# Optimization experiments

Measured on AMD Instinct MI355X. Metric: run time of the kernel, lower is better.

The kernel has to match this reference:

```python
import jax, jax.numpy as jnp
import numpy as np

B, L = 4, 40960
C = 512
DMLP = 2048
TEMP = 1e-5
EPS = 1e-5
FACTOR = 2  # Smartpool factor at layer 4


def setup_inputs() -> dict:
    key = jax.random.key(0)
    ks = jax.random.split(key, 8)

    def w(k, shape, fan_in):
        return jax.random.normal(k, shape, jnp.float32) / np.float32(np.sqrt(fan_in))

    inp = {
        "x": jax.random.normal(ks[0], (B, 1, L), jnp.float32),
        "conv0_w": w(ks[1], (C, 1, 10), 10),   "conv0_b": jnp.zeros(C, jnp.float32),
        "conv1_w": w(ks[2], (C, C, 8), C * 8), "conv1_b": jnp.zeros(C, jnp.float32),
        "conv2_w": w(ks[3], (C, C, 4), C * 4), "conv2_b": jnp.zeros(C, jnp.float32),
        "conv3_w": w(ks[4], (C, C, 4), C * 4), "conv3_b": jnp.zeros(C, jnp.float32),
        "mlp_w1": w(ks[5], (C, DMLP), C),       "mlp_b1": jnp.zeros(DMLP, jnp.float32),
        "mlp_w2": w(ks[6], (DMLP, DMLP), DMLP), "mlp_b2": jnp.zeros(DMLP, jnp.float32),
        "mlp_w3": w(ks[7], (DMLP, 1), DMLP),    "mlp_b3": jnp.zeros(1, jnp.float32),
    }
    for i in range(5):  # ChannelNorm affine params (init: ones/zeros)
        inp[f"n{i}_w"] = jnp.ones(C, jnp.float32)
        inp[f"n{i}_b"] = jnp.zeros(C, jnp.float32)
    return inp


def _conv(x, w, b, stride, pad):
    # Conv1d with padding_mode='reflect': reflect-pad then VALID conv. x: [B,C,T]
    x = jnp.pad(x, ((0, 0), (0, 0), (pad, pad)), mode="reflect")
    y = jax.lax.conv_general_dilated(x, w, (stride,), "VALID",
                                     dimension_numbers=("NCH", "OIH", "NCH"))
    return y + b[None, :, None]


def _cnorm(x, g, b):
    # ChannelNorm: normalize over channel dim with unbiased variance (torch.var default)
    m = jnp.mean(x, axis=1, keepdims=True)
    v = jnp.var(x, axis=1, keepdims=True, ddof=1)
    return (x - m) * jax.lax.rsqrt(v + EPS) * g[None, :, None] + b[None, :, None]


def _forward(x, conv0_w, conv0_b, conv1_w, conv1_b, conv2_w, conv2_b, conv3_w, conv3_b,
             n0_w, n0_b, n1_w, n1_b, n2_w, n2_b, n3_w, n3_b, n4_w, n4_b,
             mlp_w1, mlp_b1, mlp_w2, mlp_b2, mlp_w3, mlp_b3):
    h = jax.nn.relu(_cnorm(_conv(x, conv0_w, conv0_b, 5, 3), n0_w, n0_b))
    h = jax.nn.relu(_cnorm(_conv(h, conv1_w, conv1_b, 4, 2), n1_w, n1_b))
    h = jax.nn.relu(_cnorm(_conv(h, conv2_w, conv2_b, 2, 1), n2_w, n2_b))
    h = jax.nn.relu(_cnorm(_conv(h, conv3_w, conv3_b, 2, 1), n3_w, n3_b))

    f = jnp.transpose(h, (0, 2, 1))  # [B,T,C]
    T = f.shape[1]

    # importance MLP (dropout inactive in eval), exact GELU, sigmoid head
    z = jax.nn.gelu(f @ mlp_w1 + mlp_b1, approximate=False)
    z = jax.nn.gelu(z @ mlp_w2 + mlp_b2, approximate=False)
    imp = jax.nn.sigmoid((z @ mlp_w3 + mlp_b3)[..., 0]) + TEMP          # [B,T]
    imp = imp / jnp.sum(imp, axis=1, keepdims=True) * (T / FACTOR)      # sums to T/factor

    # warp: cumsum -> ramp contributions -> 2x2 [[-1,1],[1,-1]] conv = double diff
    Tn = T // FACTOR  # == round(importance_cs[0,-1])
    cs = jnp.cumsum(imp, axis=1)                                        # [B,T]
    p = jnp.maximum(cs[:, :, None] - jnp.arange(Tn, dtype=cs.dtype)[None, None, :], 0.0)  # [B,T,Tn]
    pc = jnp.pad(p, ((0, 0), (0, 0), (0, 1)))
    d = pc[:, :, :-1] - pc[:, :, 1:]                                    # diff along new-time axis
    wmat = d - jnp.pad(d, ((0, 0), (1, 0), (0, 0)))[:, :-1, :]          # diff along old-time axis, [B,T,Tn]
    pooled = jnp.einsum("btn,btc->bnc", wmat, f)                        # interp_weights @ X

    out = jnp.transpose(pooled, (0, 2, 1))                              # [B,C,Tn]
    return jax.nn.relu(_cnorm(out, n4_w, n4_b))


def reference(x, conv0_w, conv0_b, conv1_w, conv1_b, conv2_w, conv2_b, conv3_w, conv3_b,
              n0_w, n0_b, n1_w, n1_b, n2_w, n2_b, n3_w, n3_b, n4_w, n4_b,
              mlp_w1, mlp_b1, mlp_w2, mlp_b2, mlp_w3, mlp_b3):
    return _forward(x, conv0_w, conv0_b, conv1_w, conv1_b, conv2_w, conv2_b, conv3_w, conv3_b,
                    n0_w, n0_b, n1_w, n1_b, n2_w, n2_b, n3_w, n3_b, n4_w, n4_b,
                    mlp_w1, mlp_b1, mlp_w2, mlp_b2, mlp_w3, mlp_b3)
```

## Files before the change

### kernel.cpp

```cpp
#include <hip/hip_runtime.h>
#include <hip/hip_bf16.h>
#include <math.h>

#define NB 4
#define LIN 40960
#define NC 512
#define T0 8192
#define T1 2048
#define T2 1024
#define T3 512
#define TN 256
#define DM 2048
#define EPSF 1e-5f
#define TEMPF 1e-5f

typedef __attribute__((ext_vector_type(8))) short bf16x8;
typedef __attribute__((ext_vector_type(4))) float f32x4;

__device__ __forceinline__ int refl(int t, int T) {
  if (t < 0) t = -t;
  if (t >= T) t = 2 * T - 2 - t;
  return t;
}

__device__ __forceinline__ void gld16(void* lds, const void* g) {
  __builtin_amdgcn_global_load_lds((const __attribute__((address_space(1))) unsigned int*)g,
                                   (__attribute__((address_space(3))) unsigned int*)lds, 16, 0, 0);
}

__device__ __forceinline__ void blk_sum2_512(float& a, float& b, float* scratch) {
#pragma unroll
  for (int off = 32; off > 0; off >>= 1) {
    a += __shfl_down(a, off, 64);
    b += __shfl_down(b, off, 64);
  }
  int lane = threadIdx.x & 63, wid = threadIdx.x >> 6;
  __syncthreads();
  if (lane == 0) { scratch[wid] = a; scratch[8 + wid] = b; }
  __syncthreads();
  float sa = 0.f, sb = 0.f;
#pragma unroll
  for (int i = 0; i < 8; i++) { sa += scratch[i]; sb += scratch[8 + i]; }
  a = sa; b = sb;
}

__device__ __forceinline__ void add_bf8(const __hip_bfloat16* p, float* v) {
  union { uint4 u; __hip_bfloat16 h[8]; } pk;
  pk.u = *(const uint4*)p;
#pragma unroll
  for (int j = 0; j < 8; j++) v[j] += __bfloat162float(pk.h[j]);
}

template <int KT>
__device__ __forceinline__ void prep_conv_body(const float* __restrict__ w, __hip_bfloat16* __restrict__ wt,
                                               int co, float* l) {
  const float* wb = w + (size_t)co * 512 * KT;
  for (int i = threadIdx.x; i < 512 * KT; i += 256) l[i] = wb[i];
  __syncthreads();
  __hip_bfloat16* wo = wt + (size_t)co * 512 * KT;
  for (int i = threadIdx.x; i < 512 * KT; i += 256) {
    int kk = i >> 9, ci = i & 511;
    wo[i] = __float2bfloat16(l[ci * KT + kk]);
  }
}

template <int KD, int ND>
__device__ __forceinline__ void prep_mlp_body(const float* __restrict__ w, __hip_bfloat16* __restrict__ wt,
                                              int bidx, float* sbuf) {
  float(*tile)[33] = (float(*)[33])sbuf;
  int bx = bidx % (ND / 32);
  int by = bidx / (ND / 32);
  int tx = threadIdx.x & 31, ty = threadIdx.x >> 5;
#pragma unroll
  for (int i = 0; i < 32; i += 8)
    tile[ty + i][tx] = w[(size_t)(by * 32 + ty + i) * ND + bx * 32 + tx];
  __syncthreads();
#pragma unroll
  for (int i = 0; i < 32; i += 8)
    wt[(size_t)(bx * 32 + ty + i) * KD + by * 32 + tx] = __float2bfloat16(tile[tx][ty + i]);
}

__global__ __launch_bounds__(256) void k_prep(const float* c1w, const float* c2w, const float* c3w,
                                              const float* mw1, const float* mw2,
                                              __hip_bfloat16* wt1, __hip_bfloat16* wt2,
                                              __hip_bfloat16* wt3, __hip_bfloat16* wm1t,
                                              __hip_bfloat16* wm2t) {
  __shared__ float sb[4096];
  int b = blockIdx.x;
  if (b < 512) prep_conv_body<8>(c1w, wt1, b, sb);
  else if (b < 1024) prep_conv_body<4>(c2w, wt2, b - 512, sb);
  else if (b < 1536) prep_conv_body<4>(c3w, wt3, b - 1024, sb);
  else if (b < 2560) prep_mlp_body<512, 2048>(mw1, wm1t, b - 1536, sb);
  else prep_mlp_body<2048, 2048>(mw2, wm2t, b - 2560, sb);
}

__global__ __launch_bounds__(512) void k_conv0(const float* __restrict__ x, const float* __restrict__ w,
                                               const float* __restrict__ bias, const float* __restrict__ gw,
                                               const float* __restrict__ gb, __hip_bfloat16* __restrict__ out) {
  __shared__ float xv[48];
  __shared__ float tb[512 * 9];
  __shared__ float stats[16];
  int b = blockIdx.x / (T0 / 8);
  int t0 = (blockIdx.x % (T0 / 8)) * 8;
  int tid = threadIdx.x;
  if (tid < 45) xv[tid] = x[(size_t)b * LIN + refl(t0 * 5 - 3 + tid, LIN)];
  __syncthreads();
  float wk[10];
#pragma unroll
  for (int k = 0; k < 10; k++) wk[k] = w[tid * 10 + k];
  float bs = bias[tid];
  float acc[8];
#pragma unroll
  for (int tt = 0; tt < 8; tt++) {
    float a = bs;
#pragma unroll
    for (int k = 0; k < 10; k++) a += xv[tt * 5 + k] * wk[k];
    acc[tt] = a;
    tb[tid * 9 + tt] = a;
  }
  __syncthreads();
  int wave = tid >> 6, lane = tid & 63;
  float s = 0.f, q = 0.f;
#pragma unroll
  for (int j = 0; j < 8; j++) {
    float v = tb[(lane * 8 + j) * 9 + wave];
    s += v; q += v * v;
  }
#pragma unroll
  for (int off = 32; off > 0; off >>= 1) {
    s += __shfl_xor(s, off, 64);
    q += __shfl_xor(q, off, 64);
  }
  if (lane == 0) {
    float mean = s * (1.f / NC);
    float var = fmaxf((q - s * s * (1.f / NC)) * (1.f / (NC - 1)), 0.f);
    stats[wave] = mean;
    stats[8 + wave] = rsqrtf(var + EPSF);
  }
  __syncthreads();
  float gwv = gw[tid], gbv = gb[tid];
#pragma unroll
  for (int tt = 0; tt < 8; tt++) {
    float y = (acc[tt] - stats[tt]) * stats[8 + tt] * gwv + gbv;
    out[((size_t)(b * T0 + t0 + tt)) * NC + tid] = __float2bfloat16(fmaxf(y, 0.f));
  }
}

template <int MODE, int TIN_, int TOUT_, int SS, int PP, int KK, int NN, int SPLITK, int MM>
__global__ __launch_bounds__(256, 2) void k_gemm2(const __hip_bfloat16* __restrict__ A,
                                                  const __hip_bfloat16* __restrict__ Bt,
                                                  __hip_bfloat16* __restrict__ Cp) {
  __shared__ __align__(16) __hip_bfloat16 sA[2][256 * 32];
  __shared__ __align__(16) __hip_bfloat16 sB[2][128 * 32];
  const int tid = threadIdx.x;
  const int lane = tid & 63;
  const int wave = tid >> 6;
  const int wm = wave >> 1, wn = wave & 1;
  constexpr int nt = NN / 128;
  constexpr int PS = (MM / 2048) * nt;
  constexpr int KBT = KK / 32;
  const int blk = blockIdx.x;
  const int xs = blk & 7, sl = blk >> 3;
  const int sk = sl / PS, rem = sl % PS;
  const int row0 = ((rem / nt) * 8 + xs) * 256;
  const int col0 = (rem % nt) * 128;
  const int kb0 = (sk * KBT) / SPLITK, kb1 = ((sk + 1) * KBT) / SPLITK;
  const int cq = lane >> 4, cl = lane & 15;

  const char* aP[4];
  const char* bP[2];

  auto stage = [&](int kb, int buf) {
    bool recalc = (kb == kb0) || (MODE == 1 && (kb & 15) == 0);
    if (recalc) {
#pragma unroll
      for (int rr = 0; rr < 4; rr++) {
        int c = rr * 256 + tid;
        int m = c >> 2, kc = c & 3;
        int kcs = kc ^ (m & 3);
        size_t ga;
        if (MODE == 0) {
          ga = (size_t)(row0 + m) * KK + kb * 32 + kcs * 8;
        } else {
          int r = row0 + m;
          int bb = r / TOUT_;
          int t = r - bb * TOUT_;
          int k = (kb * 32) >> 9;
          int ci = ((kb * 32) & 511) + kcs * 8;
          int gt = refl(t * SS - PP + k, TIN_);
          ga = (((size_t)(bb * TIN_ + gt)) << 9) + ci;
        }
        aP[rr] = (const char*)(A + ga);
      }
#pragma unroll
      for (int rr = 0; rr < 2; rr++) {
        int c = rr * 256 + tid;
        int n = c >> 2, kc = c & 3;
        int kcs = kc ^ (n & 3);
        bP[rr] = (const char*)(Bt + (size_t)(col0 + n) * KK + kb * 32 + kcs * 8);
      }
    }
#pragma unroll
    for (int rr = 0; rr < 4; rr++) {
      int c = rr * 256 + tid;
      gld16((char*)&sA[buf][0] + c * 16, aP[rr]);
      aP[rr] += 64;
    }
#pragma unroll
    for (int rr = 0; rr < 2; rr++) {
      int c = rr * 256 + tid;
      gld16((char*)&sB[buf][0] + c * 16, bP[rr]);
      bP[rr] += 64;
    }
  };

  f32x4 acc[8][4];
  const f32x4 zz = {0.f, 0.f, 0.f, 0.f};
#pragma unroll
  for (int mi = 0; mi < 8; mi++)
#pragma unroll
    for (int ni = 0; ni < 4; ni++) acc[mi][ni] = zz;

  stage(kb0, 0);
  const int p = cq ^ (cl & 3);
  for (int kb = kb0; kb < kb1; kb++) {
    int cur = (kb - kb0) & 1;
    __syncthreads();
    if (kb + 1 < kb1) stage(kb + 1, cur ^ 1);
    const short* bA = (const short*)&sA[cur][0];
    const short* bB = (const short*)&sB[cur][0];
    bf16x8 af[8], bfr[4];
#pragma unroll
    for (int mi = 0; mi < 8; mi++)
      af[mi] = *(const bf16x8*)(bA + (wm * 128 + mi * 16 + cl) * 32 + p * 8);
#pragma unroll
    for (int ni = 0; ni < 4; ni++)
      bfr[ni] = *(const bf16x8*)(bB + (wn * 64 + ni * 16 + cl) * 32 + p * 8);
#pragma unroll
    for (int mi = 0; mi < 8; mi++)
#pragma unroll
      for (int ni = 0; ni < 4; ni++)
        acc[mi][ni] = __builtin_amdgcn_mfma_f32_16x16x32_bf16(af[mi], bfr[ni], acc[mi][ni], 0, 0, 0);
  }

#pragma unroll
  for (int mi = 0; mi < 8; mi++)
#pragma unroll
    for (int ni = 0; ni < 4; ni++)
#pragma unroll
      for (int r2 = 0; r2 < 4; r2++) {
        int row = row0 + wm * 128 + mi * 16 + cq * 4 + r2;
        int col = col0 + wn * 64 + ni * 16 + cl;
        Cp[(size_t)sk * MM * NN + (size_t)row * NN + col] = __float2bfloat16(acc[mi][ni][r2]);
      }
}

template <int MODE, int TIN_, int TOUT_, int SS, int PP, int KK, int NN, int EPI, int SPLITK, int MM>
__global__ __launch_bounds__(256, 4) void k_gemm(const __hip_bfloat16* __restrict__ A,
                                                 const __hip_bfloat16* __restrict__ Bt,
                                                 const float* __restrict__ bias,
                                                 __hip_bfloat16* __restrict__ Cout) {
  __shared__ __align__(16) __hip_bfloat16 sA[2][64 * 32];
  __shared__ __align__(16) __hip_bfloat16 sB[2][128 * 32];
  const int tid = threadIdx.x;
  const int lane = tid & 63;
  const int wave = tid >> 6;
  const int wm = wave >> 1, wn = wave & 1;
  constexpr int nt = NN / 128;
  constexpr int PS = (MM / 512) * nt;
  constexpr int KBT = KK / 32;
  const int blk = blockIdx.x;
  const int xs = blk & 7, sl = blk >> 3;
  const int sk = sl / PS, rem = sl % PS;
  const int row0 = ((rem / nt) * 8 + xs) * 64;
  const int col0 = (rem % nt) * 128;
  const int kb0 = (sk * KBT) / SPLITK, kb1 = ((sk + 1) * KBT) / SPLITK;
  const int cq = lane >> 4, cl = lane & 15;

  const char* aP;
  const char* bP[2];

  auto stage = [&](int kb, int buf) {
    bool recalc = (kb == kb0) || (MODE == 1 && (kb & 15) == 0);
    if (recalc) {
      {
        int m = tid >> 2, kc = tid & 3;
        int kcs = kc ^ (m & 3);
        size_t ga;
        if (MODE == 0) {
          ga = (size_t)(row0 + m) * KK + kb * 32 + kcs * 8;
        } else {
          int r = row0 + m;
          int bb = r / TOUT_;
          int t = r - bb * TOUT_;
          int k = (kb * 32) >> 9;
          int ci = ((kb * 32) & 511) + kcs * 8;
          int gt = refl(t * SS - PP + k, TIN_);
          ga = (((size_t)(bb * TIN_ + gt)) << 9) + ci;
        }
        aP = (const char*)(A + ga);
      }
#pragma unroll
      for (int rr = 0; rr < 2; rr++) {
        int c = rr * 256 + tid;
        int n = c >> 2, kc = c & 3;
        int kcs = kc ^ (n & 3);
        bP[rr] = (const char*)(Bt + (size_t)(col0 + n) * KK + kb * 32 + kcs * 8);
      }
    }
    gld16((char*)&sA[buf][0] + tid * 16, aP);
    aP += 64;
#pragma unroll
    for (int rr = 0; rr < 2; rr++) {
      int c = rr * 256 + tid;
      gld16((char*)&sB[buf][0] + c * 16, bP[rr]);
      bP[rr] += 64;
    }
  };

  f32x4 acc[2][4];
  const f32x4 zz = {0.f, 0.f, 0.f, 0.f};
#pragma unroll
  for (int mi = 0; mi < 2; mi++)
#pragma unroll
    for (int ni = 0; ni < 4; ni++) acc[mi][ni] = zz;

  stage(kb0, 0);
  const int p = cq ^ (cl & 3);
  for (int kb = kb0; kb < kb1; kb++) {
    int cur = (kb - kb0) & 1;
    __syncthreads();
    if (kb + 1 < kb1) stage(kb + 1, cur ^ 1);
    const short* bA = (const short*)&sA[cur][0];
    const short* bB = (const short*)&sB[cur][0];
    bf16x8 af[2], bfr[4];
#pragma unroll
    for (int mi = 0; mi < 2; mi++)
      af[mi] = *(const bf16x8*)(bA + (wm * 32 + mi * 16 + cl) * 32 + p * 8);
#pragma unroll
    for (int ni = 0; ni < 4; ni++)
      bfr[ni] = *(const bf16x8*)(bB + (wn * 64 + ni * 16 + cl) * 32 + p * 8);
#pragma unroll
    for (int mi = 0; mi < 2; mi++)
#pragma unroll
      for (int ni = 0; ni < 4; ni++)
        acc[mi][ni] = __builtin_amdgcn_mfma_f32_16x16x32_bf16(af[mi], bfr[ni], acc[mi][ni], 0, 0, 0);
  }

#pragma unroll
  for (int mi = 0; mi < 2; mi++)
#pragma unroll
    for (int ni = 0; ni < 4; ni++)
#pragma unroll
      for (int r2 = 0; r2 < 4; r2++) {
        int row = row0 + wm * 32 + mi * 16 + cq * 4 + r2;
        int col = col0 + wn * 64 + ni * 16 + cl;
        float v = acc[mi][ni][r2];
        if (EPI == 1) {
          v += bias[col];
          v = 0.5f * v * (1.f + erff(v * 0.70710678118654752f));
          Cout[(size_t)row * NN + col] = __float2bfloat16(v);
        } else {
          Cout[(size_t)sk * MM * NN + (size_t)row * NN + col] = __float2bfloat16(v);
        }
      }
}

template <int NS>
__global__ __launch_bounds__(512) void k_cnorm(const __hip_bfloat16* __restrict__ g,
                                               const float* __restrict__ cb,
                                               const float* __restrict__ gw, const float* __restrict__ gb,
                                               __hip_bfloat16* __restrict__ out, size_t stride) {
  int wave = threadIdx.x >> 6, lane = threadIdx.x & 63;
  size_t row = (size_t)blockIdx.x * 8 + wave;
  float v[8];
  {
    float4 c0 = *(const float4*)(cb + lane * 8), c1 = *(const float4*)(cb + lane * 8 + 4);
    v[0] = c0.x; v[1] = c0.y; v[2] = c0.z; v[3] = c0.w;
    v[4] = c1.x; v[5] = c1.y; v[6] = c1.z; v[7] = c1.w;
  }
#pragma unroll
  for (int s = 0; s < NS; s++) add_bf8(g + s * stride + row * NC + lane * 8, v);
  float s = 0.f, q = 0.f;
#pragma unroll
  for (int j = 0; j < 8; j++) { s += v[j]; q += v[j] * v[j]; }
#pragma unroll
  for (int off = 32; off > 0; off >>= 1) {
    s += __shfl_xor(s, off, 64);
    q += __shfl_xor(q, off, 64);
  }
  float mean = s * (1.f / NC);
  float var = fmaxf((q - s * s * (1.f / NC)) * (1.f / (NC - 1)), 0.f);
  float rstd = rsqrtf(var + EPSF);
  float4 w0 = *(const float4*)(gw + lane * 8), w1 = *(const float4*)(gw + lane * 8 + 4);
  float4 b0 = *(const float4*)(gb + lane * 8), b1 = *(const float4*)(gb + lane * 8 + 4);
  float gwv[8] = {w0.x, w0.y, w0.z, w0.w, w1.x, w1.y, w1.z, w1.w};
  float gbv[8] = {b0.x, b0.y, b0.z, b0.w, b1.x, b1.y, b1.z, b1.w};
  union { __hip_bfloat16 h[8]; uint4 u; } pk;
#pragma unroll
  for (int j = 0; j < 8; j++)
    pk.h[j] = __float2bfloat16(fmaxf((v[j] - mean) * rstd * gwv[j] + gbv[j], 0.f));
  *(uint4*)(out + row * NC + lane * 8) = pk.u;
}

template <int NS>
__global__ __launch_bounds__(256) void k_head(const __hip_bfloat16* __restrict__ g,
                                              const float* __restrict__ b2,
                                              const float* __restrict__ w3, const float* __restrict__ b3,
                                              float* __restrict__ imp) {
  __shared__ float red[4];
  int row = blockIdx.x, tid = threadIdx.x;
  int c = tid * 8;
  float v[8];
  {
    float4 x0 = *(const float4*)(b2 + c), x1 = *(const float4*)(b2 + c + 4);
    v[0] = x0.x; v[1] = x0.y; v[2] = x0.z; v[3] = x0.w;
    v[4] = x1.x; v[5] = x1.y; v[6] = x1.z; v[7] = x1.w;
  }
#pragma unroll
  for (int s = 0; s < NS; s++) add_bf8(g + (size_t)s * (2048 * DM) + (size_t)row * DM + c, v);
  float a = 0.f;
  float4 w0 = *(const float4*)(w3 + c), w1 = *(const float4*)(w3 + c + 4);
  float wv[8] = {w0.x, w0.y, w0.z, w0.w, w1.x, w1.y, w1.z, w1.w};
#pragma unroll
  for (int j = 0; j < 8; j++) {
    float z = 0.5f * v[j] * (1.f + erff(v[j] * 0.70710678118654752f));
    a += z * wv[j];
  }
#pragma unroll
  for (int off = 32; off > 0; off >>= 1) a += __shfl_down(a, off, 64);
  int lane = tid & 63, wid = tid >> 6;
  if (lane == 0) red[wid] = a;
  __syncthreads();
  if (tid == 0) {
    float s = red[0] + red[1] + red[2] + red[3] + b3[0];
    imp[row] = 1.f / (1.f + expf(-s)) + TEMPF;
  }
}

__device__ __forceinline__ float dfun(float cv, int n) {
  float d = fmaxf(cv - (float)n, 0.f);
  if (n < TN - 1) d = fminf(d, 1.f);
  return d;
}

__global__ __launch_bounds__(512) void k_poolfinal(const __hip_bfloat16* __restrict__ f,
                                                   const float* __restrict__ imp,
                                                   const float* __restrict__ gw, const float* __restrict__ gb,
                                                   float* __restrict__ out) {
  __shared__ float wt[T3];
  __shared__ float wsum[8];
  __shared__ float red[16];
  int b = blockIdx.x / TN, n = blockIdx.x % TN;
  int tid = threadIdx.x, wave = tid >> 6, lane = tid & 63;
  float own = imp[b * T3 + tid];
  float s = own;
#pragma unroll
  for (int off = 1; off < 64; off <<= 1) {
    float t = __shfl_up(s, off, 64);
    if (lane >= off) s += t;
  }
  if (lane == 63) wsum[wave] = s;
  __syncthreads();
  float prefix = 0.f, total = 0.f;
#pragma unroll
  for (int w = 0; w < 8; w++) {
    float ws_ = wsum[w];
    total += ws_;
    if (w < wave) prefix += ws_;
  }
  float scale = (float)TN / total;
  float incl = (prefix + s) * scale;
  float excl = (prefix + s - own) * scale;
  wt[tid] = dfun(incl, n) - dfun(excl, n);
  __syncthreads();
  float acc = 0.f;
  for (int t = 0; t < T3; t++) {
    float w = wt[t];
    if (w != 0.f) acc += w * __bfloat162float(f[((size_t)b * T3 + t) * NC + tid]);
  }
  float sv = acc, q = acc * acc;
  blk_sum2_512(sv, q, red);
  float mean = sv * (1.f / NC);
  float var = fmaxf((q - sv * sv * (1.f / NC)) * (1.f / (NC - 1)), 0.f);
  float y = (acc - mean) * rsqrtf(var + EPSF) * gw[tid] + gb[tid];
  out[((size_t)b * NC + tid) * TN + n] = fmaxf(y, 0.f);
}

extern "C" void kernel_launch(void* const* d_in, const int* in_sizes, int n_in,
                              void* d_out, int out_size, void* d_ws, size_t ws_size,
                              hipStream_t stream) {
  const float* x   = (const float*)d_in[0];
  const float* c0w = (const float*)d_in[1];  const float* c0b = (const float*)d_in[2];
  const float* c1w = (const float*)d_in[3];  const float* c1b = (const float*)d_in[4];
  const float* c2w = (const float*)d_in[5];  const float* c2b = (const float*)d_in[6];
  const float* c3w = (const float*)d_in[7];  const float* c3b = (const float*)d_in[8];
  const float* mw1 = (const float*)d_in[9];  const float* mb1 = (const float*)d_in[10];
  const float* mw2 = (const float*)d_in[11]; const float* mb2 = (const float*)d_in[12];
  const float* mw3 = (const float*)d_in[13]; const float* mb3 = (const float*)d_in[14];
  const float* n0w = (const float*)d_in[15]; const float* n0b = (const float*)d_in[16];
  const float* n1w = (const float*)d_in[17]; const float* n1b = (const float*)d_in[18];
  const float* n2w = (const float*)d_in[19]; const float* n2b = (const float*)d_in[20];
  const float* n3w = (const float*)d_in[21]; const float* n3b = (const float*)d_in[22];
  const float* n4w = (const float*)d_in[23]; const float* n4b = (const float*)d_in[24];

  char* base = (char*)d_ws;
  __hip_bfloat16* h0b  = (__hip_bfloat16*)(base);
  __hip_bfloat16* h1b  = (__hip_bfloat16*)(base);
  __hip_bfloat16* h2b  = (__hip_bfloat16*)(base + (8u << 20));
  __hip_bfloat16* h3b  = (__hip_bfloat16*)(base + (12u << 20));
  __hip_bfloat16* z1b  = (__hip_bfloat16*)(base + (14u << 20));
  float*          imp  = (float*)(base + (22u << 20));
  __hip_bfloat16* g    = (__hip_bfloat16*)(base + (32u << 20));
  __hip_bfloat16* wm1t = (__hip_bfloat16*)(base + (64u << 20));
  __hip_bfloat16* wt2  = (__hip_bfloat16*)(base + (66u << 20));
  __hip_bfloat16* wt3  = (__hip_bfloat16*)(base + (68u << 20));
  __hip_bfloat16* wt1  = (__hip_bfloat16*)(base + (70u << 20));
  __hip_bfloat16* wm2t = (__hip_bfloat16*)(base + (74u << 20));
  float* outp = (float*)d_out;

  k_prep<<<6656, 256, 0, stream>>>(c1w, c2w, c3w, mw1, mw2, wt1, wt2, wt3, wm1t, wm2t);
  k_conv0<<<NB * (T0 / 8), 512, 0, stream>>>(x, c0w, c0b, n0w, n0b, h0b);

  k_gemm2<1, 8192, 2048, 4, 2, 4096, 512, 4, 8192><<<512, 256, 0, stream>>>(h0b, wt1, g);
  k_cnorm<4><<<8192 / 8, 512, 0, stream>>>(g, c1b, n1w, n1b, h1b, (size_t)8192 * 512);
  k_gemm2<1, 2048, 1024, 2, 1, 2048, 512, 8, 4096><<<512, 256, 0, stream>>>(h1b, wt2, g);
  k_cnorm<8><<<4096 / 8, 512, 0, stream>>>(g, c2b, n2w, n2b, h2b, (size_t)4096 * 512);
  k_gemm<1, 1024, 512, 2, 1, 2048, 512, 0, 8, 2048><<<1024, 256, 0, stream>>>(h2b, wt3, nullptr, g);
  k_cnorm<8><<<2048 / 8, 512, 0, stream>>>(g, c3b, n3w, n3b, h3b, (size_t)2048 * 512);

  k_gemm<0, 0, 1, 0, 0, 512, 2048, 1, 1, 2048><<<512, 256, 0, stream>>>(h3b, wm1t, mb1, z1b);
  k_gemm2<0, 0, 1, 0, 0, 2048, 2048, 4, 2048><<<512, 256, 0, stream>>>(z1b, wm2t, g);

  k_head<4><<<NB * T3, 256, 0, stream>>>(g, mb2, mw3, mb3, imp);
  k_poolfinal<<<NB * TN, 512, 0, stream>>>(h3b, imp, n4w, n4b, outp);
}
```

Measured before the change: 323.7 us.

## Fuse channel-norm and MLP head into split-K GEMM tails via last-block counters

The weight prep and conv0 kernels are merged into one launch. The separate channel-norm and head kernels are removed. Each split-K GEMM now uses per-row-group atomic counters so that the last finishing block reduces the partials and applies bias, channel norm and ReLU, or the GELU/dot/sigmoid head. This cuts kernel launches and the gaps between them, at the cost of a serialized tail run by a few blocks, extra fences, and a memset for the counters.

```diff
diff --git a/kernel.cpp b/kernel.cpp
--- a/kernel.cpp
+++ b/kernel.cpp
@@ -55,10 +55,10 @@
 __device__ __forceinline__ void prep_conv_body(const float* __restrict__ w, __hip_bfloat16* __restrict__ wt,
                                                int co, float* l) {
   const float* wb = w + (size_t)co * 512 * KT;
-  for (int i = threadIdx.x; i < 512 * KT; i += 256) l[i] = wb[i];
+  for (int i = threadIdx.x; i < 512 * KT; i += 512) l[i] = wb[i];
   __syncthreads();
   __hip_bfloat16* wo = wt + (size_t)co * 512 * KT;
-  for (int i = threadIdx.x; i < 512 * KT; i += 256) {
+  for (int i = threadIdx.x; i < 512 * KT; i += 512) {
     int kk = i >> 9, ci = i & 511;
     wo[i] = __float2bfloat16(l[ci * KT + kk]);
   }
@@ -72,36 +72,23 @@
   int by = bidx / (ND / 32);
   int tx = threadIdx.x & 31, ty = threadIdx.x >> 5;
 #pragma unroll
-  for (int i = 0; i < 32; i += 8)
+  for (int i = 0; i < 32; i += 16)
     tile[ty + i][tx] = w[(size_t)(by * 32 + ty + i) * ND + bx * 32 + tx];
   __syncthreads();
 #pragma unroll
-  for (int i = 0; i < 32; i += 8)
+  for (int i = 0; i < 32; i += 16)
     wt[(size_t)(bx * 32 + ty + i) * KD + by * 32 + tx] = __float2bfloat16(tile[tx][ty + i]);
 }
 
-__global__ __launch_bounds__(256) void k_prep(const float* c1w, const float* c2w, const float* c3w,
-                                              const float* mw1, const float* mw2,
-                                              __hip_bfloat16* wt1, __hip_bfloat16* wt2,
-                                              __hip_bfloat16* wt3, __hip_bfloat16* wm1t,
-                                              __hip_bfloat16* wm2t) {
-  __shared__ float sb[4096];
-  int b = blockIdx.x;
-  if (b < 512) prep_conv_body<8>(c1w, wt1, b, sb);
-  else if (b < 1024) prep_conv_body<4>(c2w, wt2, b - 512, sb);
-  else if (b < 1536) prep_conv_body<4>(c3w, wt3, b - 1024, sb);
-  else if (b < 2560) prep_mlp_body<512, 2048>(mw1, wm1t, b - 1536, sb);
-  else prep_mlp_body<2048, 2048>(mw2, wm2t, b - 2560, sb);
-}
-
-__global__ __launch_bounds__(512) void k_conv0(const float* __restrict__ x, const float* __restrict__ w,
-                                               const float* __restrict__ bias, const float* __restrict__ gw,
-                                               const float* __restrict__ gb, __hip_bfloat16* __restrict__ out) {
-  __shared__ float xv[48];
-  __shared__ float tb[512 * 9];
-  __shared__ float stats[16];
-  int b = blockIdx.x / (T0 / 8);
-  int t0 = (blockIdx.x % (T0 / 8)) * 8;
+__device__ __forceinline__ void conv0_body(const float* __restrict__ x, const float* __restrict__ w,
+                                           const float* __restrict__ bias, const float* __restrict__ gw,
+                                           const float* __restrict__ gb, __hip_bfloat16* __restrict__ out,
+                                           int blk, float* smem) {
+  float* xv = smem;
+  float* tb = smem + 64;
+  float* stats = smem + 4672;
+  int b = blk / (T0 / 8);
+  int t0 = (blk % (T0 / 8)) * 8;
   int tid = threadIdx.x;
   if (tid < 45) xv[tid] = x[(size_t)b * LIN + refl(t0 * 5 - 3 + tid, LIN)];
   __syncthreads();
@@ -146,10 +133,33 @@
   }
 }
 
-template <int MODE, int TIN_, int TOUT_, int SS, int PP, int KK, int NN, int SPLITK, int MM>
+__global__ __launch_bounds__(512) void k_init(const float* x, const float* c0w, const float* c0b,
+                                              const float* n0w, const float* n0b, __hip_bfloat16* h0b,
+                                              const float* c1w, const float* c2w, const float* c3w,
+                                              const float* mw1, const float* mw2,
+                                              __hip_bfloat16* wt1, __hip_bfloat16* wt2,
+                                              __hip_bfloat16* wt3, __hip_bfloat16* wm1t,
+                                              __hip_bfloat16* wm2t) {
+  __shared__ float smem[4688];
+  int b = blockIdx.x;
+  if (b < 4096) conv0_body(x, c0w, c0b, n0w, n0b, h0b, b, smem);
+  else if (b < 4608) prep_conv_body<8>(c1w, wt1, b - 4096, smem);
+  else if (b < 5120) prep_conv_body<4>(c2w, wt2, b - 4608, smem);
+  else if (b < 5632) prep_conv_body<4>(c3w, wt3, b - 5120, smem);
+  else if (b < 6656) prep_mlp_body<512, 2048>(mw1, wm1t, b - 5632, smem);
+  else prep_mlp_body<2048, 2048>(mw2, wm2t, b - 6656, smem);
+}
+
+template <int MODE, int TIN_, int TOUT_, int SS, int PP, int KK, int NN, int SPLITK, int MM, int FIN>
 __global__ __launch_bounds__(256, 2) void k_gemm2(const __hip_bfloat16* __restrict__ A,
                                                   const __hip_bfloat16* __restrict__ Bt,
-                                                  __hip_bfloat16* __restrict__ Cp) {
+                                                  __hip_bfloat16* __restrict__ Cp,
+                                                  int* __restrict__ cnt,
+                                                  const float* __restrict__ f0,
+                                                  const float* __restrict__ f1,
+                                                  const float* __restrict__ f2,
+                                                  __hip_bfloat16* __restrict__ outB,
+                                                  float* __restrict__ outF) {
   __shared__ __align__(16) __hip_bfloat16 sA[2][256 * 32];
   __shared__ __align__(16) __hip_bfloat16 sB[2][128 * 32];
   const int tid = threadIdx.x;
@@ -162,7 +172,8 @@
   const int blk = blockIdx.x;
   const int xs = blk & 7, sl = blk >> 3;
   const int sk = sl / PS, rem = sl % PS;
-  const int row0 = ((rem / nt) * 8 + xs) * 256;
+  const int rg = (rem / nt) * 8 + xs;
+  const int row0 = rg * 256;
   const int col0 = (rem % nt) * 128;
   const int kb0 = (sk * KBT) / SPLITK, kb1 = ((sk + 1) * KBT) / SPLITK;
   const int cq = lane >> 4, cl = lane & 15;
@@ -253,13 +264,83 @@
         int col = col0 + wn * 64 + ni * 16 + cl;
         Cp[(size_t)sk * MM * NN + (size_t)row * NN + col] = __float2bfloat16(acc[mi][ni][r2]);
       }
-}
-
-template <int MODE, int TIN_, int TOUT_, int SS, int PP, int KK, int NN, int EPI, int SPLITK, int MM>
+
+  if constexpr (FIN != 0) {
+    __threadfence();
+    __shared__ int lf;
+    if (tid == 0) lf = (atomicAdd(cnt + rg, 1) == nt * SPLITK - 1) ? 1 : 0;
+    __syncthreads();
+    if (!lf) return;
+    __threadfence();
+    if constexpr (FIN == 1) {
+      float4 c0 = *(const float4*)(f0 + lane * 8), c1 = *(const float4*)(f0 + lane * 8 + 4);
+      float4 w0 = *(const float4*)(f1 + lane * 8), w1 = *(const float4*)(f1 + lane * 8 + 4);
+      float4 b0 = *(const float4*)(f2 + lane * 8), b1 = *(const float4*)(f2 + lane * 8 + 4);
+      float cbv[8] = {c0.x, c0.y, c0.z, c0.w, c1.x, c1.y, c1.z, c1.w};
+      float gwv[8] = {w0.x, w0.y, w0.z, w0.w, w1.x, w1.y, w1.z, w1.w};
+      float gbv[8] = {b0.x, b0.y, b0.z, b0.w, b1.x, b1.y, b1.z, b1.w};
+      for (int it = 0; it < 64; it++) {
+        int row = row0 + it * 4 + wave;
+        float v[8];
+#pragma unroll
+        for (int j = 0; j < 8; j++) v[j] = cbv[j];
+#pragma unroll
+        for (int s = 0; s < SPLITK; s++)
+          add_bf8(Cp + (size_t)s * MM * NN + (size_t)row * NN + lane * 8, v);
+        float s1 = 0.f, q = 0.f;
+#pragma unroll
+        for (int j = 0; j < 8; j++) { s1 += v[j]; q += v[j] * v[j]; }
+#pragma unroll
+        for (int off = 32; off > 0; off >>= 1) {
+          s1 += __shfl_xor(s1, off, 64);
+          q += __shfl_xor(q, off, 64);
+        }
+        float mean = s1 * (1.f / NC);
+        float var = fmaxf((q - s1 * s1 * (1.f / NC)) * (1.f / (NC - 1)), 0.f);
+        float rstd = rsqrtf(var + EPSF);
+        union { __hip_bfloat16 h[8]; uint4 u; } pk;
+#pragma unroll
+        for (int j = 0; j < 8; j++)
+          pk.h[j] = __float2bfloat16(fmaxf((v[j] - mean) * rstd * gwv[j] + gbv[j], 0.f));
+        *(uint4*)(outB + (size_t)row * NN + lane * 8) = pk.u;
+      }
+    } else {
+      for (int it = 0; it < 64; it++) {
+        int row = row0 + it * 4 + wave;
+        float a = 0.f;
+#pragma unroll
+        for (int gq = 0; gq < 4; gq++) {
+          int c = gq * 512 + lane * 8;
+          float4 x0 = *(const float4*)(f0 + c), x1 = *(const float4*)(f0 + c + 4);
+          float v[8] = {x0.x, x0.y, x0.z, x0.w, x1.x, x1.y, x1.z, x1.w};
+#pragma unroll
+          for (int s = 0; s < SPLITK; s++)
+            add_bf8(Cp + (size_t)s * MM * NN + (size_t)row * NN + c, v);
+          float4 y0 = *(const float4*)(f1 + c), y1 = *(const float4*)(f1 + c + 4);
+          float wv[8] = {y0.x, y0.y, y0.z, y0.w, y1.x, y1.y, y1.z, y1.w};
+#pragma unroll
+          for (int j = 0; j < 8; j++) {
+            float z = 0.5f * v[j] * (1.f + erff(v[j] * 0.70710678118654752f));
+            a += z * wv[j];
+          }
+        }
+#pragma unroll
+        for (int off = 32; off > 0; off >>= 1) a += __shfl_down(a, off, 64);
+        if (lane == 0) outF[row] = 1.f / (1.f + expf(-(a + f2[0]))) + TEMPF;
+      }
+    }
+  }
+}
+
+template <int MODE, int TIN_, int TOUT_, int SS, int PP, int KK, int NN, int EPI, int SPLITK, int MM, int FIN>
 __global__ __launch_bounds__(256, 4) void k_gemm(const __hip_bfloat16* __restrict__ A,
                                                  const __hip_bfloat16* __restrict__ Bt,
                                                  const float* __restrict__ bias,
-                                                 __hip_bfloat16* __restrict__ Cout) {
+                                                 __hip_bfloat16* __restrict__ Cout,
+                                                 int* __restrict__ cnt,
+                                                 const float* __restrict__ f1,
+                                                 const float* __restrict__ f2,
+                                                 __hip_bfloat16* __restrict__ outB) {
   __shared__ __align__(16) __hip_bfloat16 sA[2][64 * 32];
   __shared__ __align__(16) __hip_bfloat16 sB[2][128 * 32];
   const int tid = threadIdx.x;
@@ -272,7 +353,8 @@
   const int blk = blockIdx.x;
   const int xs = blk & 7, sl = blk >> 3;
   const int sk = sl / PS, rem = sl % PS;
-  const int row0 = ((rem / nt) * 8 + xs) * 64;
+  const int rg = (rem / nt) * 8 + xs;
+  const int row0 = rg * 64;
   const int col0 = (rem % nt) * 128;
   const int kb0 = (sk * KBT) / SPLITK, kb1 = ((sk + 1) * KBT) / SPLITK;
   const int cq = lane >> 4, cl = lane & 15;
@@ -364,77 +446,45 @@
           Cout[(size_t)sk * MM * NN + (size_t)row * NN + col] = __float2bfloat16(v);
         }
       }
-}
-
-template <int NS>
-__global__ __launch_bounds__(512) void k_cnorm(const __hip_bfloat16* __restrict__ g,
-                                               const float* __restrict__ cb,
-                                               const float* __restrict__ gw, const float* __restrict__ gb,
-                                               __hip_bfloat16* __restrict__ out, size_t stride) {
-  int wave = threadIdx.x >> 6, lane = threadIdx.x & 63;
-  size_t row = (size_t)blockIdx.x * 8 + wave;
-  float v[8];
-  {
-    float4 c0 = *(const float4*)(cb + lane * 8), c1 = *(const float4*)(cb + lane * 8 + 4);
-    v[0] = c0.x; v[1] = c0.y; v[2] = c0.z; v[3] = c0.w;
-    v[4] = c1.x; v[5] = c1.y; v[6] = c1.z; v[7] = c1.w;
-  }
-#pragma unroll
-  for (int s = 0; s < NS; s++) add_bf8(g + s * stride + row * NC + lane * 8, v);
-  float s = 0.f, q = 0.f;
-#pragma unroll
-  for (int j = 0; j < 8; j++) { s += v[j]; q += v[j] * v[j]; }
-#pragma unroll
-  for (int off = 32; off > 0; off >>= 1) {
-    s += __shfl_xor(s, off, 64);
-    q += __shfl_xor(q, off, 64);
-  }
-  float mean = s * (1.f / NC);
-  float var = fmaxf((q - s * s * (1.f / NC)) * (1.f / (NC - 1)), 0.f);
-  float rstd = rsqrtf(var + EPSF);
-  float4 w0 = *(const float4*)(gw + lane * 8), w1 = *(const float4*)(gw + lane * 8 + 4);
-  float4 b0 = *(const float4*)(gb + lane * 8), b1 = *(const float4*)(gb + lane * 8 + 4);
-  float gwv[8] = {w0.x, w0.y, w0.z, w0.w, w1.x, w1.y, w1.z, w1.w};
-  float gbv[8] = {b0.x, b0.y, b0.z, b0.w, b1.x, b1.y, b1.z, b1.w};
-  union { __hip_bfloat16 h[8]; uint4 u; } pk;
-#pragma unroll
-  for (int j = 0; j < 8; j++)
-    pk.h[j] = __float2bfloat16(fmaxf((v[j] - mean) * rstd * gwv[j] + gbv[j], 0.f));
-  *(uint4*)(out + row * NC + lane * 8) = pk.u;
-}
-
-template <int NS>
-__global__ __launch_bounds__(256) void k_head(const __hip_bfloat16* __restrict__ g,
-                                              const float* __restrict__ b2,
-                                              const float* __restrict__ w3, const float* __restrict__ b3,
-                                              float* __restrict__ imp) {
-  __shared__ float red[4];
-  int row = blockIdx.x, tid = threadIdx.x;
-  int c = tid * 8;
-  float v[8];
-  {
-    float4 x0 = *(const float4*)(b2 + c), x1 = *(const float4*)(b2 + c + 4);
-    v[0] = x0.x; v[1] = x0.y; v[2] = x0.z; v[3] = x0.w;
-    v[4] = x1.x; v[5] = x1.y; v[6] = x1.z; v[7] = x1.w;
-  }
-#pragma unroll
-  for (int s = 0; s < NS; s++) add_bf8(g + (size_t)s * (2048 * DM) + (size_t)row * DM + c, v);
-  float a = 0.f;
-  float4 w0 = *(const float4*)(w3 + c), w1 = *(const float4*)(w3 + c + 4);
-  float wv[8] = {w0.x, w0.y, w0.z, w0.w, w1.x, w1.y, w1.z, w1.w};
-#pragma unroll
-  for (int j = 0; j < 8; j++) {
-    float z = 0.5f * v[j] * (1.f + erff(v[j] * 0.70710678118654752f));
-    a += z * wv[j];
-  }
-#pragma unroll
-  for (int off = 32; off > 0; off >>= 1) a += __shfl_down(a, off, 64);
-  int lane = tid & 63, wid = tid >> 6;
-  if (lane == 0) red[wid] = a;
-  __syncthreads();
-  if (tid == 0) {
-    float s = red[0] + red[1] + red[2] + red[3] + b3[0];
-    imp[row] = 1.f / (1.f + expf(-s)) + TEMPF;
+
+  if constexpr (FIN == 1) {
+    __threadfence();
+    __shared__ int lf;
+    if (tid == 0) lf = (atomicAdd(cnt + rg, 1) == nt * SPLITK - 1) ? 1 : 0;
+    __syncthreads();
+    if (!lf) return;
+    __threadfence();
+    float4 c0 = *(const float4*)(bias + lane * 8), c1 = *(const float4*)(bias + lane * 8 + 4);
+    float4 w0 = *(const float4*)(f1 + lane * 8), w1 = *(const float4*)(f1 + lane * 8 + 4);
+    float4 b0 = *(const float4*)(f2 + lane * 8), b1 = *(const float4*)(f2 + lane * 8 + 4);
+    float cbv[8] = {c0.x, c0.y, c0.z, c0.w, c1.x, c1.y, c1.z, c1.w};
+    float gwv[8] = {w0.x, w0.y, w0.z, w0.w, w1.x, w1.y, w1.z, w1.w};
+    float gbv[8] = {b0.x, b0.y, b0.z, b0.w, b1.x, b1.y, b1.z, b1.w};
+    for (int it = 0; it < 16; it++) {
+      int row = row0 + it * 4 + wave;
+      float v[8];
+#pragma unroll
+      for (int j = 0; j < 8; j++) v[j] = cbv[j];
+#pragma unroll
+      for (int s = 0; s < SPLITK; s++)
+        add_bf8(Cout + (size_t)s * MM * NN + (size_t)row * NN + lane * 8, v);
+      float s1 = 0.f, q = 0.f;
+#pragma unroll
+      for (int j = 0; j < 8; j++) { s1 += v[j]; q += v[j] * v[j]; }
+#pragma unroll
+      for (int off = 32; off > 0; off >>= 1) {
+        s1 += __shfl_xor(s1, off, 64);
+        q += __shfl_xor(q, off, 64);
+      }
+      float mean = s1 * (1.f / NC);
+      float var = fmaxf((q - s1 * s1 * (1.f / NC)) * (1.f / (NC - 1)), 0.f);
+      float rstd = rsqrtf(var + EPSF);
+      union { __hip_bfloat16 h[8]; uint4 u; } pk;
+#pragma unroll
+      for (int j = 0; j < 8; j++)
+        pk.h[j] = __float2bfloat16(fmaxf((v[j] - mean) * rstd * gwv[j] + gbv[j], 0.f));
+      *(uint4*)(outB + (size_t)row * NN + lane * 8) = pk.u;
+    }
   }
 }
 
@@ -506,32 +556,34 @@
 
   char* base = (char*)d_ws;
   __hip_bfloat16* h0b  = (__hip_bfloat16*)(base);
-  __hip_bfloat16* h1b  = (__hip_bfloat16*)(base);
-  __hip_bfloat16* h2b  = (__hip_bfloat16*)(base + (8u << 20));
-  __hip_bfloat16* h3b  = (__hip_bfloat16*)(base + (12u << 20));
-  __hip_bfloat16* z1b  = (__hip_bfloat16*)(base + (14u << 20));
-  float*          imp  = (float*)(base + (22u << 20));
   __hip_bfloat16* g    = (__hip_bfloat16*)(base + (32u << 20));
   __hip_bfloat16* wm1t = (__hip_bfloat16*)(base + (64u << 20));
   __hip_bfloat16* wt2  = (__hip_bfloat16*)(base + (66u << 20));
   __hip_bfloat16* wt3  = (__hip_bfloat16*)(base + (68u << 20));
   __hip_bfloat16* wt1  = (__hip_bfloat16*)(base + (70u << 20));
   __hip_bfloat16* wm2t = (__hip_bfloat16*)(base + (74u << 20));
+  __hip_bfloat16* h1b  = (__hip_bfloat16*)(base + (82u << 20));
+  int*            cnt  = (int*)(base + (90u << 20));
+  __hip_bfloat16* h2b  = (__hip_bfloat16*)(base);
+  __hip_bfloat16* h3b  = (__hip_bfloat16*)(base + (4u << 20));
+  __hip_bfloat16* z1b  = (__hip_bfloat16*)(base + (6u << 20));
+  float*          imp  = (float*)(base + (14u << 20));
   float* outp = (float*)d_out;
 
-  k_prep<<<6656, 256, 0, stream>>>(c1w, c2w, c3w, mw1, mw2, wt1, wt2, wt3, wm1t, wm2t);
-  k_conv0<<<NB * (T0 / 8), 512, 0, stream>>>(x, c0w, c0b, n0w, n0b, h0b);
-
-  k_gemm2<1, 8192, 2048, 4, 2, 4096, 512, 4, 8192><<<512, 256, 0, stream>>>(h0b, wt1, g);
-  k_cnorm<4><<<8192 / 8, 512, 0, stream>>>(g, c1b, n1w, n1b, h1b, (size_t)8192 * 512);
-  k_gemm2<1, 2048, 1024, 2, 1, 2048, 512, 8, 4096><<<512, 256, 0, stream>>>(h1b, wt2, g);
-  k_cnorm<8><<<4096 / 8, 512, 0, stream>>>(g, c2b, n2w, n2b, h2b, (size_t)4096 * 512);
-  k_gemm<1, 1024, 512, 2, 1, 2048, 512, 0, 8, 2048><<<1024, 256, 0, stream>>>(h2b, wt3, nullptr, g);
-  k_cnorm<8><<<2048 / 8, 512, 0, stream>>>(g, c3b, n3w, n3b, h3b, (size_t)2048 * 512);
-
-  k_gemm<0, 0, 1, 0, 0, 512, 2048, 1, 1, 2048><<<512, 256, 0, stream>>>(h3b, wm1t, mb1, z1b);
-  k_gemm2<0, 0, 1, 0, 0, 2048, 2048, 4, 2048><<<512, 256, 0, stream>>>(z1b, wm2t, g);
-
-  k_head<4><<<NB * T3, 256, 0, stream>>>(g, mb2, mw3, mb3, imp);
+  hipMemsetAsync(cnt, 0, 512, stream);
+  k_init<<<4096 + 6656, 512, 0, stream>>>(x, c0w, c0b, n0w, n0b, h0b,
+                                          c1w, c2w, c3w, mw1, mw2, wt1, wt2, wt3, wm1t, wm2t);
+
+  k_gemm2<1, 8192, 2048, 4, 2, 4096, 512, 4, 8192, 1><<<512, 256, 0, stream>>>(
+      h0b, wt1, g, cnt + 0, c1b, n1w, n1b, h1b, nullptr);
+  k_gemm2<1, 2048, 1024, 2, 1, 2048, 512, 8, 4096, 1><<<512, 256, 0, stream>>>(
+      h1b, wt2, g, cnt + 32, c2b, n2w, n2b, h2b, nullptr);
+  k_gemm<1, 1024, 512, 2, 1, 2048, 512, 0, 8, 2048, 1><<<1024, 256, 0, stream>>>(
+      h2b, wt3, c3b, g, cnt + 48, n3w, n3b, h3b);
+  k_gemm<0, 0, 1, 0, 0, 512, 2048, 1, 1, 2048, 0><<<512, 256, 0, stream>>>(
+      h3b, wm1t, mb1, z1b, nullptr, nullptr, nullptr, nullptr);
+  k_gemm2<0, 0, 1, 0, 0, 2048, 2048, 4, 2048, 2><<<512, 256, 0, stream>>>(
+      z1b, wm2t, g, cnt + 80, mb2, mw3, mb3, nullptr, imp);
+
   k_poolfinal<<<NB * TN, 512, 0, stream>>>(h3b, imp, n4w, n4b, outp);
 }
```

Result: slower. 1.068 ms (+229.9%).

## Merge conv0 with weight prep and retile mid-size GEMMs with new split-K

Applied to the files above, without the earlier changes.

Combines conv0 and the weight-transpose prep into one 512-thread launch, removing a kernel boundary and letting the two independent jobs overlap. Adds a 128x128-tile GEMM variant used for conv2 and MLP layer 2. Split-K changes from 8 to 6 for conv2 and conv3 and from 4 to 3 for MLP2, with grids enlarged to 768 blocks to fill the device better and shrink the partial-sum buffers the norm and head kernels reduce. The merged kernel reserves conv0's shared memory for every block, and uneven split-K ranges alter the load balance across blocks.

```diff
diff --git a/kernel.cpp b/kernel.cpp
--- a/kernel.cpp
+++ b/kernel.cpp
@@ -55,10 +55,10 @@
 __device__ __forceinline__ void prep_conv_body(const float* __restrict__ w, __hip_bfloat16* __restrict__ wt,
                                                int co, float* l) {
   const float* wb = w + (size_t)co * 512 * KT;
-  for (int i = threadIdx.x; i < 512 * KT; i += 256) l[i] = wb[i];
+  for (int i = threadIdx.x; i < 512 * KT; i += 512) l[i] = wb[i];
   __syncthreads();
   __hip_bfloat16* wo = wt + (size_t)co * 512 * KT;
-  for (int i = threadIdx.x; i < 512 * KT; i += 256) {
+  for (int i = threadIdx.x; i < 512 * KT; i += 512) {
     int kk = i >> 9, ci = i & 511;
     wo[i] = __float2bfloat16(l[ci * KT + kk]);
   }
@@ -72,36 +72,23 @@
   int by = bidx / (ND / 32);
   int tx = threadIdx.x & 31, ty = threadIdx.x >> 5;
 #pragma unroll
-  for (int i = 0; i < 32; i += 8)
+  for (int i = 0; i < 32; i += 16)
     tile[ty + i][tx] = w[(size_t)(by * 32 + ty + i) * ND + bx * 32 + tx];
   __syncthreads();
 #pragma unroll
-  for (int i = 0; i < 32; i += 8)
+  for (int i = 0; i < 32; i += 16)
     wt[(size_t)(bx * 32 + ty + i) * KD + by * 32 + tx] = __float2bfloat16(tile[tx][ty + i]);
 }
 
-__global__ __launch_bounds__(256) void k_prep(const float* c1w, const float* c2w, const float* c3w,
-                                              const float* mw1, const float* mw2,
-                                              __hip_bfloat16* wt1, __hip_bfloat16* wt2,
-                                              __hip_bfloat16* wt3, __hip_bfloat16* wm1t,
-                                              __hip_bfloat16* wm2t) {
-  __shared__ float sb[4096];
-  int b = blockIdx.x;
-  if (b < 512) prep_conv_body<8>(c1w, wt1, b, sb);
-  else if (b < 1024) prep_conv_body<4>(c2w, wt2, b - 512, sb);
-  else if (b < 1536) prep_conv_body<4>(c3w, wt3, b - 1024, sb);
-  else if (b < 2560) prep_mlp_body<512, 2048>(mw1, wm1t, b - 1536, sb);
-  else prep_mlp_body<2048, 2048>(mw2, wm2t, b - 2560, sb);
-}
-
-__global__ __launch_bounds__(512) void k_conv0(const float* __restrict__ x, const float* __restrict__ w,
-                                               const float* __restrict__ bias, const float* __restrict__ gw,
-                                               const float* __restrict__ gb, __hip_bfloat16* __restrict__ out) {
-  __shared__ float xv[48];
-  __shared__ float tb[512 * 9];
-  __shared__ float stats[16];
-  int b = blockIdx.x / (T0 / 8);
-  int t0 = (blockIdx.x % (T0 / 8)) * 8;
+__device__ __forceinline__ void conv0_body(const float* __restrict__ x, const float* __restrict__ w,
+                                           const float* __restrict__ bias, const float* __restrict__ gw,
+                                           const float* __restrict__ gb, __hip_bfloat16* __restrict__ out,
+                                           int blk, float* smem) {
+  float* xv = smem;
+  float* tb = smem + 64;
+  float* stats = smem + 4672;
+  int b = blk / (T0 / 8);
+  int t0 = (blk % (T0 / 8)) * 8;
   int tid = threadIdx.x;
   if (tid < 45) xv[tid] = x[(size_t)b * LIN + refl(t0 * 5 - 3 + tid, LIN)];
   __syncthreads();
@@ -146,8 +133,25 @@
   }
 }
 
+__global__ __launch_bounds__(512) void k_init(const float* x, const float* c0w, const float* c0b,
+                                              const float* n0w, const float* n0b, __hip_bfloat16* h0b,
+                                              const float* c1w, const float* c2w, const float* c3w,
+                                              const float* mw1, const float* mw2,
+                                              __hip_bfloat16* wt1, __hip_bfloat16* wt2,
+                                              __hip_bfloat16* wt3, __hip_bfloat16* wm1t,
+                                              __hip_bfloat16* wm2t) {
+  __shared__ float smem[4688];
+  int b = blockIdx.x;
+  if (b < 4096) conv0_body(x, c0w, c0b, n0w, n0b, h0b, b, smem);
+  else if (b < 4608) prep_conv_body<8>(c1w, wt1, b - 4096, smem);
+  else if (b < 5120) prep_conv_body<4>(c2w, wt2, b - 4608, smem);
+  else if (b < 5632) prep_conv_body<4>(c3w, wt3, b - 5120, smem);
+  else if (b < 6656) prep_mlp_body<512, 2048>(mw1, wm1t, b - 5632, smem);
+  else prep_mlp_body<2048, 2048>(mw2, wm2t, b - 6656, smem);
+}
+
 template <int MODE, int TIN_, int TOUT_, int SS, int PP, int KK, int NN, int SPLITK, int MM>
-__global__ __launch_bounds__(256, 2) void k_gemm2(const __hip_bfloat16* __restrict__ A,
+__global__ __launch_bounds__(256, 2) void k_gemmA(const __hip_bfloat16* __restrict__ A,
                                                   const __hip_bfloat16* __restrict__ Bt,
                                                   __hip_bfloat16* __restrict__ Cp) {
   __shared__ __align__(16) __hip_bfloat16 sA[2][256 * 32];
@@ -202,14 +206,12 @@
     }
 #pragma unroll
     for (int rr = 0; rr < 4; rr++) {
-      int c = rr * 256 + tid;
-      gld16((char*)&sA[buf][0] + c * 16, aP[rr]);
+      gld16((char*)&sA[buf][0] + (rr * 256 + tid) * 16, aP[rr]);
       aP[rr] += 64;
     }
 #pragma unroll
     for (int rr = 0; rr < 2; rr++) {
-      int c = rr * 256 + tid;
-      gld16((char*)&sB[buf][0] + c * 16, bP[rr]);
+      gld16((char*)&sB[buf][0] + (rr * 256 + tid) * 16, bP[rr]);
       bP[rr] += 64;
     }
   };
@@ -255,11 +257,118 @@
       }
 }
 
+template <int MODE, int TIN_, int TOUT_, int SS, int PP, int KK, int NN, int SPLITK, int MM>
+__global__ __launch_bounds__(256) void k_gemmB(const __hip_bfloat16* __restrict__ A,
+                                               const __hip_bfloat16* __restrict__ Bt,
+                                               __hip_bfloat16* __restrict__ Cp) {
+  __shared__ __align__(16) __hip_bfloat16 sA[2][128 * 32];
+  __shared__ __align__(16) __hip_bfloat16 sB[2][128 * 32];
+  const int tid = threadIdx.x;
+  const int lane = tid & 63;
+  const int wave = tid >> 6;
+  const int wm = wave >> 1, wn = wave & 1;
+  constexpr int nt = NN / 128;
+  constexpr int PS = (MM / 1024) * nt;
+  constexpr int KBT = KK / 32;
+  const int blk = blockIdx.x;
+  const int xs = blk & 7, sl = blk >> 3;
+  const int sk = sl / PS, rem = sl % PS;
+  const int row0 = ((rem / nt) * 8 + xs) * 128;
+  const int col0 = (rem % nt) * 128;
+  const int kb0 = (sk * KBT) / SPLITK, kb1 = ((sk + 1) * KBT) / SPLITK;
+  const int cq = lane >> 4, cl = lane & 15;
+
+  const char* aP[2];
+  const char* bP[2];
+
+  auto stage = [&](int kb, int buf) {
+    bool recalc = (kb == kb0) || (MODE == 1 && (kb & 15) == 0);
+    if (recalc) {
+#pragma unroll
+      for (int rr = 0; rr < 2; rr++) {
+        int c = rr * 256 + tid;
+        int m = c >> 2, kc = c & 3;
+        int kcs = kc ^ (m & 3);
+        size_t ga;
+        if (MODE == 0) {
+          ga = (size_t)(row0 + m) * KK + kb * 32 + kcs * 8;
+        } else {
+          int r = row0 + m;
+          int bb = r / TOUT_;
+          int t = r - bb * TOUT_;
+          int k = (kb * 32) >> 9;
+          int ci = ((kb * 32) & 511) + kcs * 8;
+          int gt = refl(t * SS - PP + k, TIN_);
+          ga = (((size_t)(bb * TIN_ + gt)) << 9) + ci;
+        }
+        aP[rr] = (const char*)(A + ga);
+      }
+#pragma unroll
+      for (int rr = 0; rr < 2; rr++) {
+        int c = rr * 256 + tid;
+        int n = c >> 2, kc = c & 3;
+        int kcs = kc ^ (n & 3);
+        bP[rr] = (const char*)(Bt + (size_t)(col0 + n) * KK + kb * 32 + kcs * 8);
+      }
+    }
+#pragma unroll
+    for (int rr = 0; rr < 2; rr++) {
+      gld16((char*)&sA[buf][0] + (rr * 256 + tid) * 16, aP[rr]);
+      aP[rr] += 64;
+    }
+#pragma unroll
+    for (int rr = 0; rr < 2; rr++) {
+      gld16((char*)&sB[buf][0] + (rr * 256 + tid) * 16, bP[rr]);
+      bP[rr] += 64;
+    }
+  };
+
+  f32x4 acc[4][4];
+  const f32x4 zz = {0.f, 0.f, 0.f, 0.f};
+#pragma unroll
+  for (int mi = 0; mi < 4; mi++)
+#pragma unroll
+    for (int ni = 0; ni < 4; ni++) acc[mi][ni] = zz;
+
+  stage(kb0, 0);
+  const int p = cq ^ (cl & 3);
+  for (int kb = kb0; kb < kb1; kb++) {
+    int cur = (kb - kb0) & 1;
+    __syncthreads();
+    if (kb + 1 < kb1) stage(kb + 1, cur ^ 1);
+    const short* bA = (const short*)&sA[cur][0];
+    const short* bB = (const short*)&sB[cur][0];
+    bf16x8 af[4], bfr[4];
+#pragma unroll
+    for (int mi = 0; mi < 4; mi++)
+      af[mi] = *(const bf16x8*)(bA + (wm * 64 + mi * 16 + cl) * 32 + p * 8);
+#pragma unroll
+    for (int ni = 0; ni < 4; ni++)
+      bfr[ni] = *(const bf16x8*)(bB + (wn * 64 + ni * 16 + cl) * 32 + p * 8);
+#pragma unroll
+    for (int mi = 0; mi < 4; mi++)
+#pragma unroll
+      for (int ni = 0; ni < 4; ni++)
+        acc[mi][ni] = __builtin_amdgcn_mfma_f32_16x16x32_bf16(af[mi], bfr[ni], acc[mi][ni], 0, 0, 0);
+  }
+
+#pragma unroll
+  for (int mi = 0; mi < 4; mi++)
+#pragma unroll
+    for (int ni = 0; ni < 4; ni++)
+#pragma unroll
+      for (int r2 = 0; r2 < 4; r2++) {
+        int row = row0 + wm * 64 + mi * 16 + cq * 4 + r2;
+        int col = col0 + wn * 64 + ni * 16 + cl;
+        Cp[(size_t)sk * MM * NN + (size_t)row * NN + col] = __float2bfloat16(acc[mi][ni][r2]);
+      }
+}
+
 template <int MODE, int TIN_, int TOUT_, int SS, int PP, int KK, int NN, int EPI, int SPLITK, int MM>
-__global__ __launch_bounds__(256, 4) void k_gemm(const __hip_bfloat16* __restrict__ A,
-                                                 const __hip_bfloat16* __restrict__ Bt,
-                                                 const float* __restrict__ bias,
-                                                 __hip_bfloat16* __restrict__ Cout) {
+__global__ __launch_bounds__(256, 4) void k_gemmC(const __hip_bfloat16* __restrict__ A,
+                                                  const __hip_bfloat16* __restrict__ Bt,
+                                                  const float* __restrict__ bias,
+                                                  __hip_bfloat16* __restrict__ Cout) {
   __shared__ __align__(16) __hip_bfloat16 sA[2][64 * 32];
   __shared__ __align__(16) __hip_bfloat16 sB[2][128 * 32];
   const int tid = threadIdx.x;
@@ -312,8 +421,7 @@
     aP += 64;
 #pragma unroll
     for (int rr = 0; rr < 2; rr++) {
-      int c = rr * 256 + tid;
-      gld16((char*)&sB[buf][0] + c * 16, bP[rr]);
+      gld16((char*)&sB[buf][0] + (rr * 256 + tid) * 16, bP[rr]);
       bP[rr] += 64;
     }
   };
@@ -519,19 +627,18 @@
   __hip_bfloat16* wm2t = (__hip_bfloat16*)(base + (74u << 20));
   float* outp = (float*)d_out;
 
-  k_prep<<<6656, 256, 0, stream>>>(c1w, c2w, c3w, mw1, mw2, wt1, wt2, wt3, wm1t, wm2t);
-  k_conv0<<<NB * (T0 / 8), 512, 0, stream>>>(x, c0w, c0b, n0w, n0b, h0b);
-
-  k_gemm2<1, 8192, 2048, 4, 2, 4096, 512, 4, 8192><<<512, 256, 0, stream>>>(h0b, wt1, g);
+  k_init<<<4096 + 6656, 512, 0, stream>>>(x, c0w, c0b, n0w, n0b, h0b,
+                                          c1w, c2w, c3w, mw1, mw2, wt1, wt2, wt3, wm1t, wm2t);
+
+  k_gemmA<1, 8192, 2048, 4, 2, 4096, 512, 4, 8192><<<512, 256, 0, stream>>>(h0b, wt1, g);
   k_cnorm<4><<<8192 / 8, 512, 0, stream>>>(g, c1b, n1w, n1b, h1b, (size_t)8192 * 512);
-  k_gemm2<1, 2048, 1024, 2, 1, 2048, 512, 8, 4096><<<512, 256, 0, stream>>>(h1b, wt2, g);
-  k_cnorm<8><<<4096 / 8, 512, 0, stream>>>(g, c2b, n2w, n2b, h2b, (size_t)4096 * 512);
-  k_gemm<1, 1024, 512, 2, 1, 2048, 512, 0, 8, 2048><<<1024, 256, 0, stream>>>(h2b, wt3, nullptr, g);
-  k_cnorm<8><<<2048 / 8, 512, 0, stream>>>(g, c3b, n3w, n3b, h3b, (size_t)2048 * 512);
-
-  k_gemm<0, 0, 1, 0, 0, 512, 2048, 1, 1, 2048><<<512, 256, 0, stream>>>(h3b, wm1t, mb1, z1b);
-  k_gemm2<0, 0, 1, 0, 0, 2048, 2048, 4, 2048><<<512, 256, 0, stream>>>(z1b, wm2t, g);
-
-  k_head<4><<<NB * T3, 256, 0, stream>>>(g, mb2, mw3, mb3, imp);
+  k_gemmB<1, 2048, 1024, 2, 1, 2048, 512, 6, 4096><<<768, 256, 0, stream>>>(h1b, wt2, g);
+  k_cnorm<6><<<4096 / 8, 512, 0, stream>>>(g, c2b, n2w, n2b, h2b, (size_t)4096 * 512);
+  k_gemmC<1, 1024, 512, 2, 1, 2048, 512, 0, 6, 2048><<<768, 256, 0, stream>>>(h2b, wt3, c3b, g);
+  k_cnorm<6><<<2048 / 8, 512, 0, stream>>>(g, c3b, n3w, n3b, h3b, (size_t)2048 * 512);
+  k_gemmC<0, 0, 1, 0, 0, 512, 2048, 1, 1, 2048><<<512, 256, 0, stream>>>(h3b, wm1t, mb1, z1b);
+  k_gemmB<0, 0, 1, 0, 0, 2048, 2048, 3, 2048><<<768, 256, 0, stream>>>(z1b, wm2t, g);
+
+  k_head<3><<<NB * T3, 256, 0, stream>>>(g, mb2, mw3, mb3, imp);
   k_poolfinal<<<NB * TN, 512, 0, stream>>>(h3b, imp, n4w, n4b, outp);
 }
```

Result: faster. 317.2 us (-2.0%).
